# Performance work log

Hardware: AMD Instinct MI355X
Metric: run time of the kernel (lower is better)

Reference implementation:

```python
import jax, jax.numpy as jnp
import numpy as np

LN_EPS = 1e-5


def layer_norm(x, g, b):
    mu = jnp.mean(x, axis=-1, keepdims=True)
    var = jnp.mean(jnp.square(x - mu), axis=-1, keepdims=True)
    return (x - mu) * jax.lax.rsqrt(var + LN_EPS) * g + b


def setup_inputs() -> dict:
    key = jax.random.key(0)
    ks = jax.random.split(key, 8)
    N, E, D = 100000, 1000000, 128
    node_feat = jax.random.normal(ks[0], (N, D), dtype=jnp.float32)
    edge_index = jax.random.randint(ks[1], (2, E), 0, N, dtype=jnp.int64)
    s = 1.0 / np.sqrt(D)
    return {
        "node_feat": node_feat,
        "edge_index": edge_index,
        "layer_idx": 0,
        "ln1_g": jnp.ones((D,), jnp.float32),
        "ln1_b": jnp.zeros((D,), jnp.float32),
        "W_conv": jax.random.normal(ks[2], (D, D), jnp.float32) * s,
        "b_conv": jnp.zeros((D,), jnp.float32),
        "ln2_g": jnp.ones((D,), jnp.float32),
        "ln2_b": jnp.zeros((D,), jnp.float32),
        "W1": jax.random.normal(ks[3], (D, 4 * D), jnp.float32) * s,
        "b1": jnp.zeros((4 * D,), jnp.float32),
        "W2": jax.random.normal(ks[4], (4 * D, D), jnp.float32) * (0.5 * s),
        "b2": jnp.zeros((D,), jnp.float32),
    }


def reference(node_feat, edge_index, layer_idx, ln1_g, ln1_b, W_conv, b_conv,
              ln2_g, ln2_b, W1, b1, W2, b2):
    N = node_feat.shape[0]
    # DeepGCNLayer block='res+': x + conv(dropout(act(norm(x)))); dropout inert at eval
    h = jax.nn.gelu(layer_norm(node_feat, ln1_g, ln1_b), approximate=False)
    # GCNConv: symmetric-normalized aggregation with added self-loops
    hW = h @ W_conv                                         # [N, D]
    loops = jnp.arange(N, dtype=edge_index.dtype)
    src = jnp.concatenate([edge_index[0], loops])           # [E+N]
    dst = jnp.concatenate([edge_index[1], loops])
    deg = jax.ops.segment_sum(jnp.ones(src.shape, hW.dtype), dst, num_segments=N)
    dinv = jnp.where(deg > 0, jax.lax.rsqrt(deg), 0.0)
    coef = dinv[src] * dinv[dst]                            # [E+N]
    agg = jax.ops.segment_sum(hW[src] * coef[:, None], dst, num_segments=N)
    conv_feat = node_feat + agg + b_conv
    # FFN: LN -> Linear(D,4D) -> GELU -> Linear(4D,D) -> GELU, residual from node_feat
    f = layer_norm(conv_feat, ln2_g, ln2_b)
    f = jax.nn.gelu(f @ W1 + b1, approximate=False)
    f = jax.nn.gelu(f @ W2 + b2, approximate=False)
    return node_feat + f
```

## Files before the change

### kernel.cpp

```cpp
#include <hip/hip_runtime.h>
#include <math.h>


typedef _Float16 half8  __attribute__((ext_vector_type(8)));
typedef _Float16 half2v __attribute__((ext_vector_type(2)));
typedef __fp16   fp16x2 __attribute__((ext_vector_type(2)));
typedef float    floatx4 __attribute__((ext_vector_type(4)));

#define SBLK 128

__device__ __forceinline__ float gelu_f(float x){
  float x2 = x*x;
  float z  = x*(1.5957691216f + 0.07135481283f*x2);
  float e  = __expf(-z);
  return x * __builtin_amdgcn_rcpf(1.0f + e);
}
__device__ __forceinline__ unsigned pk16(float a, float b){
  fp16x2 h = __builtin_amdgcn_cvt_pkrtz(a, b);
  return __builtin_bit_cast(unsigned, h);
}
__device__ __forceinline__ float wave_reduce_sum(float v){
  #pragma unroll
  for (int off = 32; off > 0; off >>= 1) v += __shfl_xor(v, off, 64);
  return v;
}

__global__ __launch_bounds__(256) void k_hist(const int* __restrict__ ei, int* __restrict__ cnt,
                                              int E, int NB, int ESB,
    const float* __restrict__ Wc, const float* __restrict__ W1, const float* __restrict__ W2,
    _Float16* __restrict__ Wcp, _Float16* __restrict__ W1p, _Float16* __restrict__ W2p,
    const float* __restrict__ nf, const float* __restrict__ g, const float* __restrict__ b,
    _Float16* __restrict__ hs)
{
  int bid = blockIdx.x;
  if (bid < SBLK){
    __shared__ int h[2048];
    int t = threadIdx.x;
    for (int i = t; i < NB; i += 256) h[i] = 0;
    __syncthreads();
    int e0 = bid * ESB;
    int e1 = min(E, e0 + ESB);
    for (int e = e0 + t; e < e1; e += 256)
      atomicAdd(&h[ei[E + e] >> 6], 1);
    __syncthreads();
    for (int i = t; i < NB; i += 256) cnt[(size_t)bid * NB + i] = h[i];
  } else if (bid < SBLK + 72){
    int id = (bid - SBLK)*256 + threadIdx.x;
    const float* W; _Float16* P; int K, Nc, base;
    if (id < 2048)            { W = Wc; P = Wcp; K = 128; Nc = 128; base = id; }
    else if (id < 2048+8192)  { W = W1; P = W1p; K = 128; Nc = 512; base = id - 2048; }
    else                      { W = W2; P = W2p; K = 512; Nc = 128; base = id - 10240; }
    int lane = base & 63;
    int nkb  = K >> 5;
    int kb   = (base >> 6) % nkb;
    int tile = base / (nkb << 6);
    int col  = (tile << 4) + (lane & 15);
    int k0   = (kb << 5) + ((lane >> 4) << 3);
    _Float16 v[8];
    #pragma unroll
    for (int j = 0; j < 8; j++) v[j] = (_Float16)W[(size_t)(k0 + j)*Nc + col];
    *(half8*)&P[(size_t)base * 8] = *(const half8*)v;
  } else {
    int w = threadIdx.x >> 6, l = threadIdx.x & 63;
    int node = (bid - SBLK - 72)*4 + w;
    float2 x = *(const float2*)&nf[(size_t)node*128 + 2*l];
    float mu = wave_reduce_sum(x.x + x.y) * 0.0078125f;
    float d0 = x.x - mu, d1 = x.y - mu;
    float var = wave_reduce_sum(d0*d0 + d1*d1) * 0.0078125f;
    float rs = rsqrtf(var + 1e-5f);
    float y0 = gelu_f(d0*rs*g[2*l]   + b[2*l]);
    float y1 = gelu_f(d1*rs*g[2*l+1] + b[2*l+1]);
    *(unsigned*)&hs[(size_t)node*128 + 2*l] = pk16(y0, y1);
  }
}

__global__ __launch_bounds__(128) void k_scanB(int* __restrict__ cnt, int* __restrict__ total,
                                               int NB){
  __shared__ int w0sum;
  int b = blockIdx.x;
  int t = threadIdx.x, l = t & 63, w = t >> 6;
  int v = cnt[(size_t)t*NB + b];
  int x = v;
  #pragma unroll
  for (int off = 1; off < 64; off <<= 1){
    int y = __shfl_up(x, off);
    if (l >= off) x += y;
  }
  if (w == 0 && l == 63) w0sum = x;
  __syncthreads();
  int ex = x - v + (w ? w0sum : 0);
  cnt[(size_t)t*NB + b] = ex;
  if (t == 127) total[b] = ex + v;
}

__global__ __launch_bounds__(256) void k_scan2(const int* __restrict__ total,
                                               int* __restrict__ bucketStart, int NB){
  __shared__ int wsum[4];
  int t = threadIdx.x, w = t >> 6, l = t & 63;
  int vals[8];
  int sum = 0;
  #pragma unroll
  for (int j = 0; j < 8; j++){
    int idx = t*8 + j;
    vals[j] = (idx < NB) ? total[idx] : 0;
    sum += vals[j];
  }
  int x = sum;
  #pragma unroll
  for (int off = 1; off < 64; off <<= 1){
    int y = __shfl_up(x, off);
    if (l >= off) x += y;
  }
  if (l == 63) wsum[w] = x;
  __syncthreads();
  if (t == 0){
    int s = 0;
    #pragma unroll
    for (int i = 0; i < 4; i++){ int c = wsum[i]; wsum[i] = s; s += c; }
  }
  __syncthreads();
  int run = wsum[w] + x - sum;
  #pragma unroll
  for (int j = 0; j < 8; j++){
    int idx = t*8 + j;
    if (idx < NB) bucketStart[idx] = run;
    run += vals[j];
  }
  if (t == 255) bucketStart[NB] = run;
}

__global__ __launch_bounds__(256) void k_scatter(const int* __restrict__ ei,
    const int* __restrict__ cnt, const int* __restrict__ bucketStart,
    int* __restrict__ eb, int E, int NB, int ESB){
  __shared__ int cur[2048];
  int t = threadIdx.x;
  for (int i = t; i < NB; i += 256)
    cur[i] = bucketStart[i] + cnt[(size_t)blockIdx.x*NB + i];
  __syncthreads();
  int e0 = blockIdx.x*ESB, e1 = min(E, e0 + ESB);
  for (int e = e0 + t; e < e1; e += 256){
    int s = ei[e], d = ei[E + e];
    int pos = atomicAdd(&cur[d >> 6], 1);
    eb[pos] = (s << 6) | (d & 63);
  }
}

__global__ __launch_bounds__(256) void k_sort2(const int* __restrict__ eb,
    const int* __restrict__ bucketStart, int* __restrict__ eSrc,
    int* __restrict__ row_start, int* __restrict__ incount,
    float* __restrict__ dinv, int N){
  __shared__ int hcnt[64];
  __shared__ int hcur[64];
  int b = blockIdx.x, t = threadIdx.x;
  if (t < 64) hcnt[t] = 0;
  __syncthreads();
  int s0 = bucketStart[b], s1 = bucketStart[b+1];
  for (int e = s0 + t; e < s1; e += 256) atomicAdd(&hcnt[eb[e] & 63], 1);
  __syncthreads();
  if (t < 64){
    int v = hcnt[t];
    int x = v;
    #pragma unroll
    for (int off = 1; off < 64; off <<= 1){
      int y = __shfl_up(x, off);
      if (t >= off) x += y;
    }
    int ex = x - v;
    hcur[t] = ex;
    int node = (b << 6) + t;
    if (node < N){
      row_start[node] = s0 + ex;
      incount[node]   = v;
      dinv[node]      = rsqrtf((float)v + 1.0f);
    }
  }
  __syncthreads();
  for (int e = s0 + t; e < s1; e += 256){
    int v = eb[e];
    int pos = atomicAdd(&hcur[v & 63], 1);
    eSrc[s0 + pos] = v >> 6;
  }
}

__global__ __launch_bounds__(256) void k_gather(const _Float16* __restrict__ hs,
    const int* __restrict__ eSrc, const int* __restrict__ row_start,
    const int* __restrict__ incount, const float* __restrict__ dinv,
    _Float16* __restrict__ aggh, int N)
{
  int w = threadIdx.x >> 6, l = threadIdx.x & 63;
  int node = (blockIdx.x << 2) + w;
  int g  = l >> 3;
  int li = l & 7;
  float dn = dinv[node];
  int start = row_start[node], cnt = incount[node];
  float acc[16];
  #pragma unroll
  for (int i = 0; i < 16; i++) acc[i] = 0.f;
  for (int e = g; e < cnt + 1; e += 8){
    int s = (e == 0) ? node : eSrc[start + e - 1];
    float ds = dinv[s];
    const uint4* hp = (const uint4*)&hs[(size_t)s*128 + (li << 4)];
    uint4 v0 = hp[0], v1 = hp[1];
    half2v p0 = __builtin_bit_cast(half2v, v0.x), p1 = __builtin_bit_cast(half2v, v0.y);
    half2v p2 = __builtin_bit_cast(half2v, v0.z), p3 = __builtin_bit_cast(half2v, v0.w);
    half2v p4 = __builtin_bit_cast(half2v, v1.x), p5 = __builtin_bit_cast(half2v, v1.y);
    half2v p6 = __builtin_bit_cast(half2v, v1.z), p7 = __builtin_bit_cast(half2v, v1.w);
    acc[0]  = fmaf((float)p0.x, ds, acc[0]);  acc[1]  = fmaf((float)p0.y, ds, acc[1]);
    acc[2]  = fmaf((float)p1.x, ds, acc[2]);  acc[3]  = fmaf((float)p1.y, ds, acc[3]);
    acc[4]  = fmaf((float)p2.x, ds, acc[4]);  acc[5]  = fmaf((float)p2.y, ds, acc[5]);
    acc[6]  = fmaf((float)p3.x, ds, acc[6]);  acc[7]  = fmaf((float)p3.y, ds, acc[7]);
    acc[8]  = fmaf((float)p4.x, ds, acc[8]);  acc[9]  = fmaf((float)p4.y, ds, acc[9]);
    acc[10] = fmaf((float)p5.x, ds, acc[10]); acc[11] = fmaf((float)p5.y, ds, acc[11]);
    acc[12] = fmaf((float)p6.x, ds, acc[12]); acc[13] = fmaf((float)p6.y, ds, acc[13]);
    acc[14] = fmaf((float)p7.x, ds, acc[14]); acc[15] = fmaf((float)p7.y, ds, acc[15]);
  }
  #pragma unroll
  for (int i = 0; i < 16; i++){
    acc[i] += __shfl_xor(acc[i], 8);
    acc[i] += __shfl_xor(acc[i], 16);
    acc[i] += __shfl_xor(acc[i], 32);
  }
  if (l < 8){
    uint4 o0, o1;
    o0.x = pk16(dn*acc[0],  dn*acc[1]);  o0.y = pk16(dn*acc[2],  dn*acc[3]);
    o0.z = pk16(dn*acc[4],  dn*acc[5]);  o0.w = pk16(dn*acc[6],  dn*acc[7]);
    o1.x = pk16(dn*acc[8],  dn*acc[9]);  o1.y = pk16(dn*acc[10], dn*acc[11]);
    o1.z = pk16(dn*acc[12], dn*acc[13]); o1.w = pk16(dn*acc[14], dn*acc[15]);
    uint4* op = (uint4*)&aggh[(size_t)node*128 + (l << 4)];
    op[0] = o0; op[1] = o1;
  }
}

__global__ __launch_bounds__(256) void k_ffn(
    const float* __restrict__ nf, const _Float16* __restrict__ aggh,
    const _Float16* __restrict__ Wcp, const float* __restrict__ bc,
    const float* __restrict__ g2, const float* __restrict__ bl2,
    const _Float16* __restrict__ W1p, const float* __restrict__ b1,
    const _Float16* __restrict__ W2p, const float* __restrict__ b2,
    float* __restrict__ out, int N)
{
  __shared__ __align__(16) unsigned short u_s[32*520];
  int t = threadIdx.x, w = t >> 6, l = t & 63;
  int nb = blockIdx.x << 5;
  int quad = l >> 4, ln16 = l & 15;

  {
    int m = t >> 3, c0 = (t & 7) << 4;
    const uint4* src = (const uint4*)&aggh[(size_t)(nb + m)*128 + c0];
    uint4 v0 = src[0], v1 = src[1];
    uint4* dst = (uint4*)&u_s[4352 + m*136 + c0];
    dst[0] = v0; dst[1] = v1;
  }
  __syncthreads();

  {
    half8 ag[2][4];
    #pragma unroll
    for (int mt = 0; mt < 2; mt++)
      #pragma unroll
      for (int kb = 0; kb < 4; kb++)
        ag[mt][kb] = *(const half8*)&u_s[4352 + ((mt << 4) + ln16)*136 + (kb << 5) + (quad << 3)];
    const half8* Wp8 = (const half8*)Wcp;
    #pragma unroll
    for (int nt = 0; nt < 2; nt++){
      int tile = (w << 1) + nt;
      half8 bf[4];
      #pragma unroll
      for (int kb = 0; kb < 4; kb++) bf[kb] = Wp8[(size_t)((tile << 2) + kb)*64 + l];
      floatx4 acc0 = {0.f,0.f,0.f,0.f}, acc1 = {0.f,0.f,0.f,0.f};
      #pragma unroll
      for (int kb = 0; kb < 4; kb++){
        acc0 = __builtin_amdgcn_mfma_f32_16x16x32_f16(ag[0][kb], bf[kb], acc0, 0, 0, 0);
        acc1 = __builtin_amdgcn_mfma_f32_16x16x32_f16(ag[1][kb], bf[kb], acc1, 0, 0, 0);
      }
      int col = (tile << 4) + ln16;
      float bcv = bc[col];
      #pragma unroll
      for (int r = 0; r < 4; r++){
        int m0 = (quad << 2) + r;
        *(_Float16*)&u_s[m0*136 + col]        = (_Float16)(acc0[r] + bcv);
        *(_Float16*)&u_s[(m0 + 16)*136 + col] = (_Float16)(acc1[r] + bcv);
      }
    }
  }
  __syncthreads();

  float2 nfr[8];
  #pragma unroll
  for (int q = 0; q < 8; q++){
    int m = (w << 3) + q;
    unsigned pu = *(unsigned*)&u_s[m*136 + 2*l];
    half2v hp = __builtin_bit_cast(half2v, pu);
    nfr[q] = *(const float2*)&nf[(size_t)(nb + m)*128 + 2*l];
    float x0 = (float)hp.x + nfr[q].x;
    float x1 = (float)hp.y + nfr[q].y;
    float mu = wave_reduce_sum(x0 + x1) * 0.0078125f;
    float d0 = x0 - mu, d1 = x1 - mu;
    float var = wave_reduce_sum(d0*d0 + d1*d1) * 0.0078125f;
    float rs = rsqrtf(var + 1e-5f);
    float y0 = d0*rs*g2[2*l]   + bl2[2*l];
    float y1 = d1*rs*g2[2*l+1] + bl2[2*l+1];
    *(unsigned*)&u_s[m*136 + 2*l] = pk16(y0, y1);
  }
  __syncthreads();

  half8 a[2][4];
  #pragma unroll
  for (int mt = 0; mt < 2; mt++)
    #pragma unroll
    for (int kb = 0; kb < 4; kb++)
      a[mt][kb] = *(const half8*)&u_s[((mt << 4) + ln16)*136 + (kb << 5) + (quad << 3)];
  __syncthreads();

  {
    const half8* Wp8 = (const half8*)W1p;
    #pragma unroll
    for (int nt = 0; nt < 8; nt++){
      int tile = (w << 3) + nt;
      half8 bf[4];
      #pragma unroll
      for (int kb = 0; kb < 4; kb++) bf[kb] = Wp8[(size_t)((tile << 2) + kb)*64 + l];
      floatx4 acc0 = {0.f,0.f,0.f,0.f}, acc1 = {0.f,0.f,0.f,0.f};
      #pragma unroll
      for (int kb = 0; kb < 4; kb++){
        acc0 = __builtin_amdgcn_mfma_f32_16x16x32_f16(a[0][kb], bf[kb], acc0, 0, 0, 0);
        acc1 = __builtin_amdgcn_mfma_f32_16x16x32_f16(a[1][kb], bf[kb], acc1, 0, 0, 0);
      }
      int col = (tile << 4) + ln16;
      float bv = b1[col];
      #pragma unroll
      for (int r = 0; r < 4; r++){
        *(_Float16*)&u_s[((quad << 2) + r)*520 + col]      = (_Float16)gelu_f(acc0[r] + bv);
        *(_Float16*)&u_s[(16 + (quad << 2) + r)*520 + col] = (_Float16)gelu_f(acc1[r] + bv);
      }
    }
  }
  __syncthreads();

  floatx4 acc00 = {0.f,0.f,0.f,0.f}, acc01 = {0.f,0.f,0.f,0.f};
  floatx4 acc10 = {0.f,0.f,0.f,0.f}, acc11 = {0.f,0.f,0.f,0.f};
  int tile0 = (w << 1), tile1 = tile0 + 1;
  {
    const half8* Wp8 = (const half8*)W2p;
    for (int kb = 0; kb < 16; kb++){
      half8 a0 = *(const half8*)&u_s[ln16*520        + (kb << 5) + (quad << 3)];
      half8 a1 = *(const half8*)&u_s[(16 + ln16)*520 + (kb << 5) + (quad << 3)];
      half8 b0  = Wp8[(size_t)((tile0 << 4) + kb)*64 + l];
      half8 b1v = Wp8[(size_t)((tile1 << 4) + kb)*64 + l];
      acc00 = __builtin_amdgcn_mfma_f32_16x16x32_f16(a0, b0,  acc00, 0, 0, 0);
      acc01 = __builtin_amdgcn_mfma_f32_16x16x32_f16(a0, b1v, acc01, 0, 0, 0);
      acc10 = __builtin_amdgcn_mfma_f32_16x16x32_f16(a1, b0,  acc10, 0, 0, 0);
      acc11 = __builtin_amdgcn_mfma_f32_16x16x32_f16(a1, b1v, acc11, 0, 0, 0);
    }
  }
  __syncthreads();

  {
    float* fs = (float*)u_s;
    int col0 = (tile0 << 4) + ln16, col1 = (tile1 << 4) + ln16;
    float bv0 = b2[col0], bv1 = b2[col1];
    #pragma unroll
    for (int r = 0; r < 4; r++){
      int m0 = (quad << 2) + r;
      fs[m0*132 + col0]        = gelu_f(acc00[r] + bv0);
      fs[m0*132 + col1]        = gelu_f(acc01[r] + bv1);
      fs[(m0 + 16)*132 + col0] = gelu_f(acc10[r] + bv0);
      fs[(m0 + 16)*132 + col1] = gelu_f(acc11[r] + bv1);
    }
  }
  __syncthreads();

  {
    const float* fs = (const float*)u_s;
    #pragma unroll
    for (int q = 0; q < 8; q++){
      int m = (w << 3) + q;
      float2 o;
      o.x = nfr[q].x + fs[m*132 + 2*l];
      o.y = nfr[q].y + fs[m*132 + 2*l + 1];
      *(float2*)&out[(size_t)(nb + m)*128 + 2*l] = o;
    }
  }
}

extern "C" void kernel_launch(void* const* d_in, const int* in_sizes, int n_in,
                              void* d_out, int out_size, void* d_ws, size_t ws_size,
                              hipStream_t stream) {
  const float* nf   = (const float*)d_in[0];
  const int*   ei   = (const int*)  d_in[1];
  const float* ln1g = (const float*)d_in[3];
  const float* ln1b = (const float*)d_in[4];
  const float* Wc   = (const float*)d_in[5];
  const float* bc   = (const float*)d_in[6];
  const float* ln2g = (const float*)d_in[7];
  const float* ln2b = (const float*)d_in[8];
  const float* W1   = (const float*)d_in[9];
  const float* b1   = (const float*)d_in[10];
  const float* W2   = (const float*)d_in[11];
  const float* b2   = (const float*)d_in[12];
  float* out = (float*)d_out;

  int N = in_sizes[0] / 128;
  int E = in_sizes[1] / 2;
  int NB  = (N + 63) >> 6;
  int ESB = (E + SBLK - 1) / SBLK;

  char* ws = (char*)d_ws;
  _Float16* hs   = (_Float16*)ws;
  _Float16* aggh = (_Float16*)(ws + (size_t)N*128*2);
  char* p = ws + (size_t)N*128*4;
  p = (char*)(((size_t)p + 15) & ~(size_t)15);
  int*   cnt         = (int*)p;   p += (size_t)SBLK*NB*4;
  int*   total       = (int*)p;   p += (size_t)NB*4;
  int*   bucketStart = (int*)p;   p += (size_t)(NB+1)*4;
  float* dinv        = (float*)p; p += (size_t)N*4;
  int*   incount     = (int*)p;   p += (size_t)N*4;
  int*   row_start   = (int*)p;   p += (size_t)N*4;
  int*   eb          = (int*)p;   p += (size_t)E*4;
  int*   eSrc        = (int*)p;   p += (size_t)E*4;
  p = (char*)(((size_t)p + 15) & ~(size_t)15);
  _Float16* Wcp = (_Float16*)p; p += (size_t)2048*8*2;
  _Float16* W1p = (_Float16*)p; p += (size_t)8192*8*2;
  _Float16* W2p = (_Float16*)p; p += (size_t)8192*8*2;

  k_hist   <<<SBLK + 72 + N/4, 256, 0, stream>>>(ei, cnt, E, NB, ESB,
                                                 Wc, W1, W2, Wcp, W1p, W2p,
                                                 nf, ln1g, ln1b, hs);
  k_scanB  <<<NB, 128, 0, stream>>>(cnt, total, NB);
  k_scan2  <<<1, 256, 0, stream>>>(total, bucketStart, NB);
  k_scatter<<<SBLK, 256, 0, stream>>>(ei, cnt, bucketStart, eb, E, NB, ESB);
  k_sort2  <<<NB, 256, 0, stream>>>(eb, bucketStart, eSrc, row_start, incount, dinv, N);

  k_gather <<<N/4, 256, 0, stream>>>(hs, eSrc, row_start, incount, dinv, aggh, N);
  k_ffn    <<<N/32, 256, 0, stream>>>(nf, aggh, Wcp, bc, ln2g, ln2b, W1p, b1, W2p, b2, out, N);
}
```

Before: 286.8 us.

## Fuse bucket scans via last-block pattern and swizzle FFN LDS layout

Result: slower. 408.4 us (+42.4%).

```diff
diff --git a/kernel.cpp b/kernel.cpp
--- a/kernel.cpp
+++ b/kernel.cpp
@@ -30,12 +30,13 @@
     const float* __restrict__ Wc, const float* __restrict__ W1, const float* __restrict__ W2,
     _Float16* __restrict__ Wcp, _Float16* __restrict__ W1p, _Float16* __restrict__ W2p,
     const float* __restrict__ nf, const float* __restrict__ g, const float* __restrict__ b,
-    _Float16* __restrict__ hs)
+    _Float16* __restrict__ hs, int* __restrict__ done)
 {
   int bid = blockIdx.x;
   if (bid < SBLK){
     __shared__ int h[2048];
     int t = threadIdx.x;
+    if (bid == 0 && t == 0) *done = 0;
     for (int i = t; i < NB; i += 256) h[i] = 0;
     __syncthreads();
     int e0 = bid * ESB;
@@ -74,9 +75,11 @@
   }
 }
 
-__global__ __launch_bounds__(128) void k_scanB(int* __restrict__ cnt, int* __restrict__ total,
-                                               int NB){
+__global__ __launch_bounds__(128) void kBC(int* __restrict__ cnt, int* __restrict__ total,
+                                           int* __restrict__ bucketStart, int NB, int E,
+                                           int* __restrict__ done){
   __shared__ int w0sum;
+  __shared__ int amLast;
   int b = blockIdx.x;
   int t = threadIdx.x, l = t & 63, w = t >> 6;
   int v = cnt[(size_t)t*NB + b];
@@ -90,43 +93,34 @@
   __syncthreads();
   int ex = x - v + (w ? w0sum : 0);
   cnt[(size_t)t*NB + b] = ex;
-  if (t == 127) total[b] = ex + v;
-}
-
-__global__ __launch_bounds__(256) void k_scan2(const int* __restrict__ total,
-                                               int* __restrict__ bucketStart, int NB){
-  __shared__ int wsum[4];
-  int t = threadIdx.x, w = t >> 6, l = t & 63;
-  int vals[8];
-  int sum = 0;
-  #pragma unroll
-  for (int j = 0; j < 8; j++){
-    int idx = t*8 + j;
-    vals[j] = (idx < NB) ? total[idx] : 0;
-    sum += vals[j];
-  }
-  int x = sum;
-  #pragma unroll
-  for (int off = 1; off < 64; off <<= 1){
-    int y = __shfl_up(x, off);
-    if (l >= off) x += y;
-  }
-  if (l == 63) wsum[w] = x;
-  __syncthreads();
-  if (t == 0){
-    int s = 0;
-    #pragma unroll
-    for (int i = 0; i < 4; i++){ int c = wsum[i]; wsum[i] = s; s += c; }
-  }
-  __syncthreads();
-  int run = wsum[w] + x - sum;
-  #pragma unroll
-  for (int j = 0; j < 8; j++){
-    int idx = t*8 + j;
-    if (idx < NB) bucketStart[idx] = run;
-    run += vals[j];
-  }
-  if (t == 255) bucketStart[NB] = run;
+  if (t == 127) atomicExch(&total[b], ex + v);
+  __threadfence();
+  __syncthreads();
+  if (t == 0) amLast = (atomicAdd(done, 1) == NB - 1);
+  __syncthreads();
+  if (!amLast) return;
+
+  __shared__ int carrySh;
+  if (t == 0) carrySh = 0;
+  __syncthreads();
+  for (int base = 0; base < NB; base += 128){
+    int idx = base + t;
+    int tv = (idx < NB) ? atomicAdd(&total[idx], 0) : 0;
+    int xx = tv;
+    #pragma unroll
+    for (int off = 1; off < 64; off <<= 1){
+      int y = __shfl_up(xx, off);
+      if (l >= off) xx += y;
+    }
+    if (w == 0 && l == 63) w0sum = xx;
+    __syncthreads();
+    int ex2 = xx - tv + (w ? w0sum : 0);
+    if (idx < NB) bucketStart[idx] = carrySh + ex2;
+    __syncthreads();
+    if (t == 127) carrySh += ex2 + tv;
+    __syncthreads();
+  }
+  if (t == 0) bucketStart[NB] = carrySh;
 }
 
 __global__ __launch_bounds__(256) void k_scatter(const int* __restrict__ ei,
@@ -239,7 +233,7 @@
     const _Float16* __restrict__ W2p, const float* __restrict__ b2,
     float* __restrict__ out, int N)
 {
-  __shared__ __align__(16) unsigned short u_s[32*520];
+  __shared__ __align__(16) unsigned short u_s[16384];
   int t = threadIdx.x, w = t >> 6, l = t & 63;
   int nb = blockIdx.x << 5;
   int quad = l >> 4, ln16 = l & 15;
@@ -330,8 +324,10 @@
       float bv = b1[col];
       #pragma unroll
       for (int r = 0; r < 4; r++){
-        *(_Float16*)&u_s[((quad << 2) + r)*520 + col]      = (_Float16)gelu_f(acc0[r] + bv);
-        *(_Float16*)&u_s[(16 + (quad << 2) + r)*520 + col] = (_Float16)gelu_f(acc1[r] + bv);
+        int r0 = (quad << 2) + r;
+        int r1 = 16 + r0;
+        *(_Float16*)&u_s[r0*512 + (col ^ ((r0 & 7) << 3))] = (_Float16)gelu_f(acc0[r] + bv);
+        *(_Float16*)&u_s[r1*512 + (col ^ ((r1 & 7) << 3))] = (_Float16)gelu_f(acc1[r] + bv);
       }
     }
   }
@@ -342,9 +338,11 @@
   int tile0 = (w << 1), tile1 = tile0 + 1;
   {
     const half8* Wp8 = (const half8*)W2p;
+    int swz = (ln16 & 7) << 3;
     for (int kb = 0; kb < 16; kb++){
-      half8 a0 = *(const half8*)&u_s[ln16*520        + (kb << 5) + (quad << 3)];
-      half8 a1 = *(const half8*)&u_s[(16 + ln16)*520 + (kb << 5) + (quad << 3)];
+      int c0 = (kb << 5) + (quad << 3);
+      half8 a0 = *(const half8*)&u_s[ln16*512        + (c0 ^ swz)];
+      half8 a1 = *(const half8*)&u_s[(16 + ln16)*512 + (c0 ^ swz)];
       half8 b0  = Wp8[(size_t)((tile0 << 4) + kb)*64 + l];
       half8 b1v = Wp8[(size_t)((tile1 << 4) + kb)*64 + l];
       acc00 = __builtin_amdgcn_mfma_f32_16x16x32_f16(a0, b0,  acc00, 0, 0, 0);
@@ -418,6 +416,7 @@
   int*   row_start   = (int*)p;   p += (size_t)N*4;
   int*   eb          = (int*)p;   p += (size_t)E*4;
   int*   eSrc        = (int*)p;   p += (size_t)E*4;
+  int*   done        = (int*)p;   p += 16;
   p = (char*)(((size_t)p + 15) & ~(size_t)15);
   _Float16* Wcp = (_Float16*)p; p += (size_t)2048*8*2;
   _Float16* W1p = (_Float16*)p; p += (size_t)8192*8*2;
@@ -425,9 +424,8 @@
 
   k_hist   <<<SBLK + 72 + N/4, 256, 0, stream>>>(ei, cnt, E, NB, ESB,
                                                  Wc, W1, W2, Wcp, W1p, W2p,
-                                                 nf, ln1g, ln1b, hs);
-  k_scanB  <<<NB, 128, 0, stream>>>(cnt, total, NB);
-  k_scan2  <<<1, 256, 0, stream>>>(total, bucketStart, NB);
+                                                 nf, ln1g, ln1b, hs, done);
+  kBC      <<<NB, 128, 0, stream>>>(cnt, total, bucketStart, NB, E, done);
   k_scatter<<<SBLK, 256, 0, stream>>>(ei, cnt, bucketStart, eb, E, NB, ESB);
   k_sort2  <<<NB, 256, 0, stream>>>(eb, bucketStart, eSrc, row_start, incount, dinv, N);
 
```
